# Performance work log

Measured on AMD Instinct MI355X. Metric: run time of the kernel, lower is better.

The kernel has to match this reference:

```python
import jax, jax.numpy as jnp
import numpy as np
from math import log

N = 100000          # num_nodes
D = 128             # emb_dimension
NEG = 5             # negatives per node
LR = 0.025
NCE_BIAS = log(N)
NCE_NEG_BIAS = log(N / NEG)
LUT_SIZE = 1202     # len(arange(-6.01, 6.01, 0.01))


def make_lookup_table():
    t = jax.nn.sigmoid(jnp.arange(-6.01, 6.01, 0.01, dtype=jnp.float32))
    t = t.at[0].set(0.0).at[-1].set(1.0)
    return t


def fast_sigmoid(score, lookup_table):
    idx = jnp.floor((score + 6.01) / 0.01).astype(jnp.int32)
    idx = jnp.clip(idx, 0, LUT_SIZE - 1)  # guard float rounding at +/-6
    return jnp.take(lookup_table, idx)


def setup_inputs() -> dict:
    key = jax.random.key(0)
    k1, k2, k3, k4, k5 = jax.random.split(key, 5)
    W = jax.random.uniform(k1, (N, D), dtype=jnp.float32, minval=-0.5, maxval=0.5)
    lookup_table = make_lookup_table()
    idx_pos_u = jax.random.randint(k2, (N,), 0, N)
    idx_pos_v = jax.random.randint(k3, (N,), 0, N)
    idx_neg_u = jnp.repeat(idx_pos_u, NEG)  # matches sample_index: same u repeated per negative
    idx_neg_v = jax.random.randint(k5, (N * NEG,), 0, N)
    return {"W": W, "lookup_table": lookup_table,
            "idx_pos_u": idx_pos_u, "idx_pos_v": idx_pos_v,
            "idx_neg_u": idx_neg_u, "idx_neg_v": idx_neg_v}


def reference(W, lookup_table, idx_pos_u, idx_pos_v, idx_neg_u, idx_neg_v):
    # ---- positive pairs: gather, dot, LUT-sigmoid, scatter-add ----
    emb_pos_u = W[idx_pos_u]                       # [N, D]
    emb_pos_v = W[idx_pos_v]                       # [N, D]
    pos_score = jnp.sum(emb_pos_u * emb_pos_v, axis=1) - NCE_BIAS
    pos_score = jnp.clip(pos_score, -6.0, 6.0)
    score = ((1.0 - fast_sigmoid(pos_score, lookup_table)) * LR)[:, None]
    W = W.at[idx_pos_u].add(score * emb_pos_v)
    W = W.at[idx_pos_v].add(score * emb_pos_u)
    # ---- negative pairs: gathers read the UPDATED table (as in torch code) ----
    emb_neg_u = W[idx_neg_u]                       # [N*NEG, D]
    emb_neg_v = W[idx_neg_v]                       # [N*NEG, D]
    neg_score = jnp.sum(emb_neg_u * emb_neg_v, axis=1) - NCE_NEG_BIAS
    neg_score = jnp.clip(neg_score, -6.0, 6.0)
    score = (0.0 - fast_sigmoid(neg_score, lookup_table) * LR)[:, None]
    W = W.at[idx_neg_u].add(score * emb_neg_v)
    W = W.at[idx_neg_v].add(score * emb_neg_u)
    return W
```

## Files before the change

### kernel.cpp

```cpp
#include <hip/hip_runtime.h>
#include <hip/hip_bf16.h>

#define D 128
#define LR 0.025f
#define NCE_BIAS 11.512925464970229f
#define NCE_NEG_BIAS 9.903487552536127f
#define LUT_SIZE 1202

__device__ __forceinline__ float wave_allreduce(float x) {
    #pragma unroll
    for (int m = 32; m >= 1; m >>= 1) x += __shfl_xor(x, m, 64);
    return x;
}

__device__ __forceinline__ float fast_sig(float x) {
    x = fminf(fmaxf(x, -6.0f), 6.0f) - 0.005f;
    float e = __expf(-x);
    return __builtin_amdgcn_rcpf(1.0f + e);
}

__device__ __forceinline__ float fast_sig_lut(float s, const float* __restrict__ lut) {
    s = fminf(fmaxf(s, -6.0f), 6.0f);
    int idx = (int)floorf((s + 6.01f) / 0.01f);
    idx = min(max(idx, 0), LUT_SIZE - 1);
    return lut[idx];
}

__device__ __forceinline__ unsigned int bf16_rne(float f) {
    unsigned int u = __float_as_uint(f);
    return (u + 0x7FFFu + ((u >> 16) & 1u)) >> 16;
}

__global__ __launch_bounds__(256) void conv_kernel(
    const float* __restrict__ W, unsigned short* __restrict__ w16, int n32)
{
    int g = blockIdx.x * 256 + threadIdx.x;
    if (g >= n32) return;
    float4 v = ((const float4*)W)[g];
    uint2 h;
    h.x = bf16_rne(v.x) | (bf16_rne(v.y) << 16);
    h.y = bf16_rne(v.z) | (bf16_rne(v.w) << 16);
    ((uint2*)w16)[g] = h;
}

__global__ __launch_bounds__(256) void hist_kernel(
    const int* __restrict__ ipu, const int* __restrict__ ipv,
    const int* __restrict__ inv,
    int Np, int Nn, int NEG, int2* __restrict__ cnt2)
{
    int t = blockIdx.x * 256 + threadIdx.x;
    if (t < Np) {
        atomicAdd((unsigned long long*)&cnt2[ipu[t]],
                  1ull + ((unsigned long long)NEG << 32));
        atomicAdd(&cnt2[ipv[t]].x, 1);
    } else if (t < Np + Nn) {
        int k = t - Np;
        atomicAdd(&cnt2[inv[k]].y, 1);
    }
}

__global__ __launch_bounds__(256) void scan_local2(
    const int2* __restrict__ cnt2, int* __restrict__ off_p, int* __restrict__ off_n,
    int* __restrict__ bsp, int* __restrict__ bsn, int n)
{
    __shared__ int shp[256], shn[256];
    int g = blockIdx.x * 256 + threadIdx.x;
    int2 x = (g < n) ? cnt2[g] : make_int2(0, 0);
    shp[threadIdx.x] = x.x;
    shn[threadIdx.x] = x.y;
    __syncthreads();
    #pragma unroll
    for (int d = 1; d < 256; d <<= 1) {
        int tp = (threadIdx.x >= d) ? shp[threadIdx.x - d] : 0;
        int tn = (threadIdx.x >= d) ? shn[threadIdx.x - d] : 0;
        __syncthreads();
        shp[threadIdx.x] += tp;
        shn[threadIdx.x] += tn;
        __syncthreads();
    }
    if (g < n) {
        off_p[g] = shp[threadIdx.x] - x.x;
        off_n[g] = shn[threadIdx.x] - x.y;
    }
    if (threadIdx.x == 255) {
        bsp[blockIdx.x] = shp[255];
        bsn[blockIdx.x] = shn[255];
    }
}

__device__ __forceinline__ void scan_one(int* b, int nb) {
    __shared__ int sh[256];
    __shared__ int carry_s;
    if (threadIdx.x == 0) carry_s = 0;
    __syncthreads();
    for (int c = 0; c < nb; c += 256) {
        int i = c + threadIdx.x;
        int x = (i < nb) ? b[i] : 0;
        sh[threadIdx.x] = x;
        __syncthreads();
        for (int d = 1; d < 256; d <<= 1) {
            int t = (threadIdx.x >= d) ? sh[threadIdx.x - d] : 0;
            __syncthreads();
            sh[threadIdx.x] += t;
            __syncthreads();
        }
        int carry = carry_s;
        if (i < nb) b[i] = sh[threadIdx.x] - x + carry;
        __syncthreads();
        if (threadIdx.x == 0) carry_s = carry + sh[255];
        __syncthreads();
    }
}

__global__ __launch_bounds__(256) void scan_bsum2(int* __restrict__ bsp, int* __restrict__ bsn, int nb)
{
    scan_one(bsp, nb);
    __syncthreads();
    scan_one(bsn, nb);
}

__global__ __launch_bounds__(256) void add_base2(
    int* __restrict__ off_p, int* __restrict__ off_n, int2* __restrict__ cur2,
    const int* __restrict__ bsp, const int* __restrict__ bsn, int n)
{
    int g = blockIdx.x * 256 + threadIdx.x;
    if (g < n) {
        int vp = off_p[g] + bsp[blockIdx.x];
        int vn = off_n[g] + bsn[blockIdx.x];
        off_p[g] = vp;
        off_n[g] = vn;
        cur2[g] = make_int2(vp, vn);
    }
}

__global__ __launch_bounds__(256) void fill_kernel(
    const int* __restrict__ ipu, const int* __restrict__ ipv,
    const int* __restrict__ inu, const int* __restrict__ inv,
    int Np, int Nn, int NEG,
    int2* __restrict__ cur2, int* __restrict__ ent_p, int* __restrict__ ent_n)
{
    int t = blockIdx.x * 256 + threadIdx.x;
    if (t < Np) {
        int u = ipu[t], v = ipv[t];
        unsigned long long pk = atomicAdd((unsigned long long*)&cur2[u],
                                          1ull + ((unsigned long long)NEG << 32));
        int slot_pu = (int)(pk & 0xFFFFFFFFull);
        int slot_nu = (int)(pk >> 32);
        ent_p[slot_pu] = v;
        for (int j = 0; j < NEG; ++j)
            ent_n[slot_nu + j] = inv[(size_t)NEG * t + j];
        ent_p[atomicAdd(&cur2[v].x, 1)] = u;
    } else if (t < Np + Nn) {
        int k = t - Np;
        ent_n[atomicAdd(&cur2[inv[k]].y, 1)] = inu[k];
    }
}

template<bool EMIT16>
__global__ __launch_bounds__(256) void update_kernel(
    const float* __restrict__ baseSrc,
    const unsigned short* __restrict__ partnerH,
    float* __restrict__ dst, unsigned short* __restrict__ dst16,
    const int* __restrict__ offArr, const int* __restrict__ endArr2, int comp,
    const int* __restrict__ entries, int N, float bias, float cpos)
{
    int gtid = blockIdx.x * 256 + threadIdx.x;
    int node = gtid >> 5;
    int hl   = threadIdx.x & 31;
    if (node >= N) return;

    float4 base = ((const float4*)baseSrc)[(size_t)node * 32 + hl];
    float ax = 0.0f, ay = 0.0f, az = 0.0f, aw = 0.0f;

    int beg = offArr[node];
    int len = endArr2[2 * node + comp] - beg;
    const uint2* ph = (const uint2*)partnerH;

    if (len > 0) {
        int gcount = (len + 3) >> 2;
        int en[4];
        uint2 rc[4];
        #pragma unroll
        for (int i = 0; i < 4; ++i) {
            int t = min(i, len - 1);
            rc[i] = ph[(size_t)entries[beg + t] * 32 + hl];
        }
        #pragma unroll
        for (int i = 0; i < 4; ++i) {
            int t = min(4 + i, len - 1);
            en[i] = entries[beg + t];
        }
        for (int g = 0; g < gcount; ++g) {
            uint2 rn[4];
            #pragma unroll
            for (int i = 0; i < 4; ++i) rn[i] = ph[(size_t)en[i] * 32 + hl];
            int en2[4];
            #pragma unroll
            for (int i = 0; i < 4; ++i) {
                int t = (g + 2) * 4 + i;
                t = (t < len) ? t : (len - 1);
                en2[i] = entries[beg + t];
            }
            float4 r[4];
            float d[4];
            #pragma unroll
            for (int i = 0; i < 4; ++i) {
                r[i].x = __uint_as_float(rc[i].x << 16);
                r[i].y = __uint_as_float(rc[i].x & 0xFFFF0000u);
                r[i].z = __uint_as_float(rc[i].y << 16);
                r[i].w = __uint_as_float(rc[i].y & 0xFFFF0000u);
                d[i] = r[i].x * base.x + r[i].y * base.y + r[i].z * base.z + r[i].w * base.w;
            }
            #pragma unroll
            for (int m = 16; m >= 1; m >>= 1) {
                #pragma unroll
                for (int i = 0; i < 4; ++i) d[i] += __shfl_xor(d[i], m, 64);
            }
            #pragma unroll
            for (int i = 0; i < 4; ++i) {
                float s = (g * 4 + i < len) ? (cpos - fast_sig(d[i] - bias)) * LR : 0.0f;
                ax += s * r[i].x;
                ay += s * r[i].y;
                az += s * r[i].z;
                aw += s * r[i].w;
            }
            #pragma unroll
            for (int i = 0; i < 4; ++i) { rc[i] = rn[i]; en[i] = en2[i]; }
        }
    }
    float4 o = make_float4(base.x + ax, base.y + ay, base.z + az, base.w + aw);
    ((float4*)dst)[(size_t)node * 32 + hl] = o;
    if (EMIT16) {
        uint2 h;
        h.x = bf16_rne(o.x) | (bf16_rne(o.y) << 16);
        h.y = bf16_rne(o.z) | (bf16_rne(o.w) << 16);
        ((uint2*)dst16)[(size_t)node * 32 + hl] = h;
    }
}

__global__ __launch_bounds__(256) void pos_kernel(
    const float* __restrict__ Worig, float* __restrict__ W,
    const float* __restrict__ lut,
    const int* __restrict__ idx_u, const int* __restrict__ idx_v, int n)
{
    int wave = (int)((blockIdx.x * blockDim.x + threadIdx.x) >> 6);
    int lane = threadIdx.x & 63;
    if (wave >= n) return;
    int u = idx_u[wave];
    int v = idx_v[wave];
    float2 eu = ((const float2*)(Worig + (size_t)u * D))[lane];
    float2 ev = ((const float2*)(Worig + (size_t)v * D))[lane];
    float dot = wave_allreduce(eu.x * ev.x + eu.y * ev.y);
    float s = (1.0f - fast_sig_lut(dot - NCE_BIAS, lut)) * LR;
    float* wu = W + (size_t)u * D;
    float* wv = W + (size_t)v * D;
    atomicAdd(&wu[2 * lane],     s * ev.x);
    atomicAdd(&wu[2 * lane + 1], s * ev.y);
    atomicAdd(&wv[2 * lane],     s * eu.x);
    atomicAdd(&wv[2 * lane + 1], s * eu.y);
}

__global__ __launch_bounds__(256) void neg_kernel(
    const float* __restrict__ Wsnap, float* __restrict__ W,
    const float* __restrict__ lut,
    const int* __restrict__ idx_u, const int* __restrict__ idx_v, int n, int neg)
{
    int wave = (int)((blockIdx.x * blockDim.x + threadIdx.x) >> 6);
    int lane = threadIdx.x & 63;
    if (wave >= n) return;
    int u = idx_u[wave * neg];
    float2 eu = ((const float2*)(Wsnap + (size_t)u * D))[lane];
    float dux = 0.0f, duy = 0.0f;
    for (int j = 0; j < neg; ++j) {
        int v = idx_v[wave * neg + j];
        float2 ev = ((const float2*)(Wsnap + (size_t)v * D))[lane];
        float dot = wave_allreduce(eu.x * ev.x + eu.y * ev.y);
        float s = -fast_sig_lut(dot - NCE_NEG_BIAS, lut) * LR;
        dux += s * ev.x;
        duy += s * ev.y;
        float* wv = W + (size_t)v * D;
        atomicAdd(&wv[2 * lane],     s * eu.x);
        atomicAdd(&wv[2 * lane + 1], s * eu.y);
    }
    float* wu = W + (size_t)u * D;
    atomicAdd(&wu[2 * lane],     dux);
    atomicAdd(&wu[2 * lane + 1], duy);
}

extern "C" void kernel_launch(void* const* d_in, const int* in_sizes, int n_in,
                              void* d_out, int out_size, void* d_ws, size_t ws_size,
                              hipStream_t stream) {
    const float* W   = (const float*)d_in[0];
    const float* lut = (const float*)d_in[1];
    const int* ipu   = (const int*)d_in[2];
    const int* ipv   = (const int*)d_in[3];
    const int* inu   = (const int*)d_in[4];
    const int* inv   = (const int*)d_in[5];
    float* out = (float*)d_out;

    const int N  = in_sizes[0] / D;
    const int Np = in_sizes[2];
    const int Nn = in_sizes[4];
    const int NEG = Nn / Np;
    const size_t WB = (size_t)N * D * sizeof(float);
    const int nb = (N + 255) / 256;
    const int n_entp = 2 * Np;
    const int n_entn = NEG * Np + Nn;

    size_t need = (size_t)N * D * 2 * 2
                + (size_t)n_entp * 4 + (size_t)n_entn * 4
                + (size_t)N * 8 * 2 + (size_t)N * 4 * 2
                + (size_t)nb * 4 * 2 + 64;

    if (ws_size >= need) {
        char* p = (char*)d_ws;
        unsigned short* w16W = (unsigned short*)p; p += (size_t)N * D * 2;
        unsigned short* w16P = (unsigned short*)p; p += (size_t)N * D * 2;
        int*  ent_p = (int*)p;  p += (size_t)n_entp * 4;
        int*  ent_n = (int*)p;  p += (size_t)n_entn * 4;
        int2* cnt2  = (int2*)p; p += (size_t)N * 8;
        int2* cur2  = (int2*)p; p += (size_t)N * 8;
        int*  off_p = (int*)p;  p += (size_t)N * 4;
        int*  off_n = (int*)p;  p += (size_t)N * 4;
        int*  bsp   = (int*)p;  p += (size_t)nb * 4;
        int*  bsn   = (int*)p;

        hipMemsetAsync(cnt2, 0, (size_t)N * 8, stream);
        int n32 = N * 32;
        conv_kernel<<<(n32 + 255) / 256, 256, 0, stream>>>(W, w16W, n32);
        int tot = Np + Nn;
        hist_kernel<<<(tot + 255) / 256, 256, 0, stream>>>(ipu, ipv, inv, Np, Nn, NEG, cnt2);
        scan_local2<<<nb, 256, 0, stream>>>(cnt2, off_p, off_n, bsp, bsn, N);
        scan_bsum2<<<1, 256, 0, stream>>>(bsp, bsn, nb);
        add_base2<<<nb, 256, 0, stream>>>(off_p, off_n, cur2, bsp, bsn, N);
        fill_kernel<<<(tot + 255) / 256, 256, 0, stream>>>(ipu, ipv, inu, inv, Np, Nn, NEG,
                                                           cur2, ent_p, ent_n);

        int ublocks = (n32 + 255) / 256;
        update_kernel<true><<<ublocks, 256, 0, stream>>>(
            W, w16W, out, w16P, off_p, (const int*)cur2, 0, ent_p, N, NCE_BIAS, 1.0f);
        update_kernel<false><<<ublocks, 256, 0, stream>>>(
            out, w16P, out, (unsigned short*)nullptr, off_n, (const int*)cur2, 1, ent_n,
            N, NCE_NEG_BIAS, 0.0f);
    } else {
        float* snap = (float*)d_ws;
        hipMemcpyAsync(out, W, WB, hipMemcpyDeviceToDevice, stream);
        int blocks = (Np * 64 + 255) / 256;
        pos_kernel<<<blocks, 256, 0, stream>>>(W, out, lut, ipu, ipv, Np);
        hipMemcpyAsync(snap, out, WB, hipMemcpyDeviceToDevice, stream);
        neg_kernel<<<blocks, 256, 0, stream>>>(snap, out, lut, inu, inv, Np, NEG);
    }
}
```

Baseline: 272.4 us.

## Fuse bf16 conversion with histogram, parallelize block scans, shuffle-broadcast entry indices

Merges the fp32-to-bf16 conversion and the degree histogram into one prep kernel, which removes a launch. The two block-sum scans now run in separate blocks instead of one after the other. In the update kernel, each half-wave loads 32 entry indices cooperatively and broadcasts them with shuffles, replacing per-lane scalar index loads, and it double-buffers the partner rows across A/B register sets. This cuts redundant index memory traffic, at the cost of added shuffle work and more complex control flow.

```diff
diff --git a/kernel.cpp b/kernel.cpp
--- a/kernel.cpp
+++ b/kernel.cpp
@@ -31,24 +31,20 @@
     return (u + 0x7FFFu + ((u >> 16) & 1u)) >> 16;
 }
 
-__global__ __launch_bounds__(256) void conv_kernel(
-    const float* __restrict__ W, unsigned short* __restrict__ w16, int n32)
-{
-    int g = blockIdx.x * 256 + threadIdx.x;
-    if (g >= n32) return;
-    float4 v = ((const float4*)W)[g];
-    uint2 h;
-    h.x = bf16_rne(v.x) | (bf16_rne(v.y) << 16);
-    h.y = bf16_rne(v.z) | (bf16_rne(v.w) << 16);
-    ((uint2*)w16)[g] = h;
-}
-
-__global__ __launch_bounds__(256) void hist_kernel(
+__global__ __launch_bounds__(256) void prep_kernel(
+    const float* __restrict__ W, unsigned short* __restrict__ w16, int n32,
     const int* __restrict__ ipu, const int* __restrict__ ipv,
     const int* __restrict__ inv,
     int Np, int Nn, int NEG, int2* __restrict__ cnt2)
 {
     int t = blockIdx.x * 256 + threadIdx.x;
+    if (t < n32) {
+        float4 v = ((const float4*)W)[t];
+        uint2 h;
+        h.x = bf16_rne(v.x) | (bf16_rne(v.y) << 16);
+        h.y = bf16_rne(v.z) | (bf16_rne(v.w) << 16);
+        ((uint2*)w16)[t] = h;
+    }
     if (t < Np) {
         atomicAdd((unsigned long long*)&cnt2[ipu[t]],
                   1ull + ((unsigned long long)NEG << 32));
@@ -114,9 +110,7 @@
 
 __global__ __launch_bounds__(256) void scan_bsum2(int* __restrict__ bsp, int* __restrict__ bsn, int nb)
 {
-    scan_one(bsp, nb);
-    __syncthreads();
-    scan_one(bsn, nb);
+    scan_one(blockIdx.x == 0 ? bsp : bsn, nb);
 }
 
 __global__ __launch_bounds__(256) void add_base2(
@@ -156,6 +150,29 @@
     }
 }
 
+
+__device__ __forceinline__ void advance_chunk(
+    const int* __restrict__ entries, int beg, int len, int t,
+    int& c0, int& e, int hl)
+{
+    int c0n = (min(t * 4, len - 1) >> 5) << 5;
+    if (c0n > c0) {
+        c0 = c0n;
+        e = entries[beg + min(c0 + hl, len - 1)];
+    }
+}
+
+__device__ __forceinline__ void load_rows(
+    const uint2* __restrict__ ph, int hl, int e, int c0, int t, int len, uint2 r[4])
+{
+    #pragma unroll
+    for (int i = 0; i < 4; ++i) {
+        int idx = min(t * 4 + i, len - 1) - c0;
+        int p = __shfl(e, idx, 32);
+        r[i] = ph[(size_t)p * 32 + hl];
+    }
+}
+
 template<bool EMIT16>
 __global__ __launch_bounds__(256) void update_kernel(
     const float* __restrict__ baseSrc,
@@ -177,56 +194,52 @@
     const uint2* ph = (const uint2*)partnerH;
 
     if (len > 0) {
-        int gcount = (len + 3) >> 2;
-        int en[4];
-        uint2 rc[4];
-        #pragma unroll
-        for (int i = 0; i < 4; ++i) {
-            int t = min(i, len - 1);
-            rc[i] = ph[(size_t)entries[beg + t] * 32 + hl];
+        int G = (len + 3) >> 2;
+        int c0 = 0;
+        int e = entries[beg + min(hl, len - 1)];
+        uint2 A[4], B[4];
+        load_rows(ph, hl, e, c0, 0, len, A);
+        load_rows(ph, hl, e, c0, 1, len, B);
+
+        #define STEP(BUF, G_IDX)                                               \
+        {                                                                      \
+            int gg = (G_IDX);                                                  \
+            float4 r[4]; float d[4];                                           \
+            _Pragma("unroll")                                                  \
+            for (int i = 0; i < 4; ++i) {                                      \
+                r[i].x = __uint_as_float(BUF[i].x << 16);                      \
+                r[i].y = __uint_as_float(BUF[i].x & 0xFFFF0000u);              \
+                r[i].z = __uint_as_float(BUF[i].y << 16);                      \
+                r[i].w = __uint_as_float(BUF[i].y & 0xFFFF0000u);              \
+                d[i] = r[i].x * base.x + r[i].y * base.y                       \
+                     + r[i].z * base.z + r[i].w * base.w;                      \
+            }                                                                  \
+            _Pragma("unroll")                                                  \
+            for (int m = 16; m >= 1; m >>= 1) {                                \
+                _Pragma("unroll")                                              \
+                for (int i = 0; i < 4; ++i) d[i] += __shfl_xor(d[i], m, 64);   \
+            }                                                                  \
+            _Pragma("unroll")                                                  \
+            for (int i = 0; i < 4; ++i) {                                      \
+                float s = (gg * 4 + i < len)                                   \
+                        ? (cpos - fast_sig(d[i] - bias)) * LR : 0.0f;          \
+                ax += s * r[i].x;                                              \
+                ay += s * r[i].y;                                              \
+                az += s * r[i].z;                                              \
+                aw += s * r[i].w;                                              \
+            }                                                                  \
+            int t2 = gg + 2;                                                   \
+            if (t2 < G) {                                                      \
+                advance_chunk(entries, beg, len, t2, c0, e, hl);               \
+                load_rows(ph, hl, e, c0, t2, len, BUF);                        \
+            }                                                                  \
         }
-        #pragma unroll
-        for (int i = 0; i < 4; ++i) {
-            int t = min(4 + i, len - 1);
-            en[i] = entries[beg + t];
+
+        for (int g = 0; g < G; g += 2) {
+            STEP(A, g);
+            if (g + 1 < G) STEP(B, g + 1);
         }
-        for (int g = 0; g < gcount; ++g) {
-            uint2 rn[4];
-            #pragma unroll
-            for (int i = 0; i < 4; ++i) rn[i] = ph[(size_t)en[i] * 32 + hl];
-            int en2[4];
-            #pragma unroll
-            for (int i = 0; i < 4; ++i) {
-                int t = (g + 2) * 4 + i;
-                t = (t < len) ? t : (len - 1);
-                en2[i] = entries[beg + t];
-            }
-            float4 r[4];
-            float d[4];
-            #pragma unroll
-            for (int i = 0; i < 4; ++i) {
-                r[i].x = __uint_as_float(rc[i].x << 16);
-                r[i].y = __uint_as_float(rc[i].x & 0xFFFF0000u);
-                r[i].z = __uint_as_float(rc[i].y << 16);
-                r[i].w = __uint_as_float(rc[i].y & 0xFFFF0000u);
-                d[i] = r[i].x * base.x + r[i].y * base.y + r[i].z * base.z + r[i].w * base.w;
-            }
-            #pragma unroll
-            for (int m = 16; m >= 1; m >>= 1) {
-                #pragma unroll
-                for (int i = 0; i < 4; ++i) d[i] += __shfl_xor(d[i], m, 64);
-            }
-            #pragma unroll
-            for (int i = 0; i < 4; ++i) {
-                float s = (g * 4 + i < len) ? (cpos - fast_sig(d[i] - bias)) * LR : 0.0f;
-                ax += s * r[i].x;
-                ay += s * r[i].y;
-                az += s * r[i].z;
-                aw += s * r[i].w;
-            }
-            #pragma unroll
-            for (int i = 0; i < 4; ++i) { rc[i] = rn[i]; en[i] = en2[i]; }
-        }
+        #undef STEP
     }
     float4 o = make_float4(base.x + ax, base.y + ay, base.z + az, base.w + aw);
     ((float4*)dst)[(size_t)node * 32 + hl] = o;
@@ -327,11 +340,11 @@
 
         hipMemsetAsync(cnt2, 0, (size_t)N * 8, stream);
         int n32 = N * 32;
-        conv_kernel<<<(n32 + 255) / 256, 256, 0, stream>>>(W, w16W, n32);
         int tot = Np + Nn;
-        hist_kernel<<<(tot + 255) / 256, 256, 0, stream>>>(ipu, ipv, inv, Np, Nn, NEG, cnt2);
+        int pgrid = (max(n32, tot) + 255) / 256;
+        prep_kernel<<<pgrid, 256, 0, stream>>>(W, w16W, n32, ipu, ipv, inv, Np, Nn, NEG, cnt2);
         scan_local2<<<nb, 256, 0, stream>>>(cnt2, off_p, off_n, bsp, bsn, N);
-        scan_bsum2<<<1, 256, 0, stream>>>(bsp, bsn, nb);
+        scan_bsum2<<<2, 256, 0, stream>>>(bsp, bsn, nb);
         add_base2<<<nb, 256, 0, stream>>>(off_p, off_n, cur2, bsp, bsn, N);
         fill_kernel<<<(tot + 255) / 256, 256, 0, stream>>>(ipu, ipv, inu, inv, Np, Nn, NEG,
                                                            cur2, ent_p, ent_n);
```

Result: no change. 275.8 us (+1.2%).
